# Optimization experiments

Measured on AMD Instinct MI355X. Metric: run time of the kernel, lower is better.

## Reference

```python
import jax, jax.numpy as jnp
import numpy as np

B, T, S, H, E, V, M = 64, 59, 32, 512, 300, 34004, 1024  # batch, dec steps, enc len, hidden, embed, vocab, enc dim (bi)


def setup_inputs() -> dict:
    key = jax.random.key(0)
    ks = jax.random.split(key, 14)
    w = lambda k, sh, sc=0.05: jax.random.normal(k, sh, jnp.float32) * sc
    return dict(
        dec_input=jax.random.randint(ks[0], (B, T), 0, V),
        enc_output=w(ks[1], (B, S, M), 1.0),
        enc_h=w(ks[2], (B, H), 1.0),
        enc_c=w(ks[3], (B, H), 1.0),
        embedding=w(ks[4], (V, E)),
        Wx=w(ks[5], (E + H, 4 * H)),   # LSTM input kernel (input = [emb; prev_attention])
        Uh=w(ks[6], (H, 4 * H)),       # LSTM recurrent kernel
        b=jnp.zeros((4 * H,), jnp.float32),
        Wm=w(ks[7], (M, H)),           # Bahdanau memory layer
        Wq=w(ks[8], (H, H)),           # Bahdanau query layer
        v=w(ks[9], (H,)),              # Bahdanau attention vector
        Wa=w(ks[10], (H + M, H)),      # attention_layer (Dense, no bias)
        Wf=w(ks[11], (H, V)),          # output projection to vocab
        bf=jnp.zeros((V,), jnp.float32),
    )


def reference(dec_input, enc_output, enc_h, enc_c, embedding, Wx, Uh, b, Wm, Wq, v, Wa, Wf, bf):
    # Precompute attention keys once: [B,S,H]
    keys = jnp.einsum('bsm,mh->bsh', enc_output, Wm)
    emb = embedding[dec_input]            # [B,T,E] teacher-forced inputs
    emb_t = jnp.swapaxes(emb, 0, 1)       # [T,B,E]

    def step(carry, x_t):
        h, c, attn = carry
        x = jnp.concatenate([x_t, attn], axis=-1)          # [B,E+H]
        z = x @ Wx + h @ Uh + b                            # [B,4H]
        i, f, g, o = jnp.split(z, 4, axis=-1)              # keras gate order i,f,c,o
        c2 = jax.nn.sigmoid(f) * c + jax.nn.sigmoid(i) * jnp.tanh(g)
        h2 = jax.nn.sigmoid(o) * jnp.tanh(c2)
        # Bahdanau attention: score = v . tanh(keys + Wq q)
        q = h2 @ Wq                                        # [B,H]
        scores = jnp.einsum('h,bsh->bs', v, jnp.tanh(keys + q[:, None, :]))
        align = jax.nn.softmax(scores, axis=-1)            # full memory (seq_len == S)
        ctx = jnp.einsum('bs,bsm->bm', align, enc_output)  # [B,M]
        attn2 = jnp.concatenate([h2, ctx], axis=-1) @ Wa   # attention_layer, [B,H]
        logits = attn2 @ Wf + bf                           # [B,V]
        return (h2, c2, attn2), logits

    init = (enc_h, enc_c, jnp.zeros((B, H), enc_h.dtype))
    _, logits = jax.lax.scan(step, init, emb_t)            # [T,B,V]
    return jnp.swapaxes(logits, 0, 1)                      # [B,T,V]
```

## Files before the change

### kernel.cpp

```cpp
#include <hip/hip_runtime.h>
#include <hip/hip_bf16.h>
#include <hip/hip_fp16.h>
#include <cstdint>
#include <cstddef>

typedef unsigned short u16;
typedef unsigned long long u64;
typedef short s8v __attribute__((ext_vector_type(8)));
typedef float f4v __attribute__((ext_vector_type(4)));
typedef _Float16 f16x2 __attribute__((ext_vector_type(2)));

#define DI __device__ __forceinline__

#if defined(__has_builtin)
#  if __has_builtin(__builtin_amdgcn_fdot2)
#    define HAS_FDOT2 1
#  endif
#endif

DI u16 f2bf(float f){ unsigned u = __float_as_uint(f); u += 0x7fffu + ((u>>16)&1u); return (u16)(u>>16); }
DI float bf2f(u16 h){ return __uint_as_float(((unsigned)h)<<16); }
DI int ocol(int pc){ return ((pc>>3)&3)*512 + (pc>>5)*8 + (pc&7); }
DI int ocol2(int s){ int pc = (s & ~31) | ((s&3)<<3) | ((s>>2)&7); return ocol(pc); }
DI int pc2slot(int pc){ return (pc & ~31) | ((pc&7)<<2) | ((pc>>3)&3); }
DI float sigm(float x){ x = fminf(fmaxf(x,-30.f),30.f); return 1.f/(1.f+__expf(-x)); }
DI float tanhx(float x){ x = fminf(fmaxf(x,-15.f),15.f); float e = __expf(-2.f*x); return (1.f-e)/(1.f+e); }
DI uint4 packh8(const u16* h){
  uint4 r; r.x=(unsigned)h[0]|((unsigned)h[1]<<16); r.y=(unsigned)h[2]|((unsigned)h[3]<<16);
  r.z=(unsigned)h[4]|((unsigned)h[5]<<16); r.w=(unsigned)h[6]|((unsigned)h[7]<<16); return r;
}
DI s8v u4s8(uint4 u){ union{uint4 a; s8v b;} t; t.a=u; return t.b; }

DI float qdot(unsigned w, f16x2 hv, float acc){
#ifdef HAS_FDOT2
  f16x2 wv; __builtin_memcpy(&wv, &w, 4);
  return __builtin_amdgcn_fdot2(wv, hv, acc, false);
#else
  __half2 hp = *reinterpret_cast<const __half2*>(&w);
  return acc + (float)hv[0]*__half2float(hp.x) + (float)hv[1]*__half2float(hp.y);
#endif
}

DI unsigned cohld32(const void* p){
  return __hip_atomic_load((const unsigned*)p, __ATOMIC_RELAXED, __HIP_MEMORY_SCOPE_AGENT);
}
DI u64 cohld64(const void* p){
  return __hip_atomic_load((const u64*)p, __ATOMIC_RELAXED, __HIP_MEMORY_SCOPE_AGENT);
}
DI f4v cohldf4(const float* p){
  u64 lo = cohld64(p);
  u64 hi = cohld64(p + 2);
  f4v r;
  r[0]=__uint_as_float((unsigned)lo); r[1]=__uint_as_float((unsigned)(lo>>32));
  r[2]=__uint_as_float((unsigned)hi); r[3]=__uint_as_float((unsigned)(hi>>32));
  return r;
}
DI void cohst32(void* p, unsigned v){
  __hip_atomic_store((unsigned*)p, v, __ATOMIC_RELAXED, __HIP_MEMORY_SCOPE_AGENT);
}
DI void cohst64(void* p, u64 v){
  __hip_atomic_store((u64*)p, v, __ATOMIC_RELAXED, __HIP_MEMORY_SCOPE_AGENT);
}

__global__ __launch_bounds__(256) void k_build(
    const float* __restrict__ bb, const float* __restrict__ eh, const float* __restrict__ ec,
    const int* __restrict__ dec, const float* __restrict__ enc, const float* __restrict__ emb,
    const float* __restrict__ Wx, const float* __restrict__ Uh, const float* __restrict__ Wm,
    const float* __restrict__ Wq, const float* __restrict__ Wa, const float* __restrict__ Wf,
    float* __restrict__ bp, float* __restrict__ h2X, float* __restrict__ cst,
    float* __restrict__ ctxX, unsigned* __restrict__ flags,
    u16* __restrict__ hhi, u16* __restrict__ hlo, u16* __restrict__ encB,
    u16* __restrict__ wq2, u16* __restrict__ wmT, u16* __restrict__ waT,
    u16* __restrict__ wxtpT, u16* __restrict__ wxaT, u16* __restrict__ buhT,
    u16* __restrict__ waA, u16* __restrict__ embB, u16* __restrict__ WfT){
  __shared__ u16 T[64*72];
  int lb = blockIdx.x, tid = threadIdx.x;
  if (lb < 638){
    int i = lb*256 + tid;
    if (i < 2048) bp[i] = bb[ocol2(i)];
    else if (i < 2048+32768) h2X[i-2048] = eh[i-2048];
    else if (i < 2048+65536) cst[i-34816] = ec[i-34816];
    else if (i < 2048+131072) ctxX[i-67584] = 0.f;
    else if (i < 2048+131072+30208) flags[i-133120] = 0u;
  } else if (lb < 1022){
    int i = (lb-638)*256 + tid; if (i >= 64*1536) return;
    int c = i % 1536;
    float f = (c < 512) ? eh[(i/1536)*512 + c] : 0.f;
    u16 hi = f2bf(f);
    hhi[i] = hi;
    hlo[i] = (c < 512) ? f2bf(f - bf2f(hi)) : (u16)0;
  } else if (lb < 2046){
    int g = (lb-1022)*256 + tid; if (g >= 262144) return;
    const float4* p = (const float4*)(enc + (size_t)g*8);
    float4 a = p[0], b = p[1];
    u16 h[8] = {f2bf(a.x),f2bf(a.y),f2bf(a.z),f2bf(a.w),f2bf(b.x),f2bf(b.y),f2bf(b.z),f2bf(b.w)};
    *(uint4*)&encB[(size_t)g*8] = packh8(h);
  } else if (lb < 3070){
    int g = (lb-2046)*256 + tid; if (g >= 262144) return;
    int h = g>>9, c = g&511;
    __half hf = __float2half(Wq[g]);
    wq2[(size_t)(h>>1)*1024 + (c<<1) + (h&1)] = *reinterpret_cast<u16*>(&hf);
  } else if (lb < 3326){
    int g = (lb-3070)*256 + tid; if (g >= 512*128) return;
    int hcol = g/128, o = g%128;
    u16 h[8];
    #pragma unroll
    for(int j=0;j<8;++j){ int m = o*8+j; h[j]=f2bf(Wm[(size_t)m*512 + hcol]); }
    *(uint4*)&wmT[(size_t)hcol*1024 + o*8] = packh8(h);
  } else if (lb < 3710){
    int g = (lb-3326)*256 + tid; if (g >= 512*192) return;
    int c = g/192, o = g%192;
    u16 h[8];
    #pragma unroll
    for(int j=0;j<8;++j){ int k = o*8+j; h[j]=f2bf(Wa[(size_t)k*512 + c]); }
    *(uint4*)&waT[(size_t)c*1536 + o*8] = packh8(h);
  } else if (lb < 4030){
    int g = (lb-3710)*256 + tid; if (g >= 2048*40) return;
    int pc = g/40, o = g%40; int oc = ocol2(pc);
    u16 h[8];
    #pragma unroll
    for(int j=0;j<8;++j){ int e = o*8+j; float f = (e<300)? Wx[(size_t)e*2048 + oc] : 0.f; h[j]=f2bf(f); }
    *(uint4*)&wxtpT[(size_t)pc*320 + o*8] = packh8(h);
  } else if (lb < 5566){
    int g = (lb-4030)*256 + tid; if (g >= 2048*192) return;
    int pc = g/192, o = g%192; int oc = ocol(pc);
    u16 h[8];
    #pragma unroll
    for(int j=0;j<8;++j){
      int kp = o*8+j; int seg = kp>>9; int jd = kp&511;
      float f = Wx[(size_t)(300+jd)*2048 + oc];
      u16 hi = f2bf(f);
      h[j] = (seg==2) ? f2bf(f - bf2f(hi)) : hi;
    }
    *(uint4*)&wxaT[(size_t)pc*1536 + o*8] = packh8(h);
  } else if (lb < 6590){
    int g = (lb-5566)*256 + tid; if (g >= 2048*128) return;
    int pc = g/128, o = g%128; int oc = ocol(pc);
    u16 h[8];
    #pragma unroll
    for(int j=0;j<8;++j){
      int kp = o*8+j; int r = kp&511;
      float f = Uh[(size_t)r*2048 + oc];
      u16 hi = f2bf(f);
      h[j] = (kp<512) ? hi : f2bf(f - bf2f(hi));
    }
    *(uint4*)&buhT[(size_t)pc*1024 + o*8] = packh8(h);
  } else if (lb < 7742){
    int g = (lb-6590)*256 + tid; if (g >= 1536*192) return;
    int r = g/192, o = g%192;
    u16 h[8];
    #pragma unroll
    for(int j=0;j<8;++j){
      int kp = o*8+j; int seg = kp>>9; int jd = kp&511;
      float f = Wa[(size_t)r*512 + jd];
      u16 hi = f2bf(f);
      h[j] = (seg==1) ? f2bf(f - bf2f(hi)) : hi;
    }
    *(uint4*)&waA[(size_t)r*1536 + o*8] = packh8(h);
  } else if (lb < 8332){
    int g = (lb-7742)*256 + tid; if (g >= 3776*40) return;
    int row = g/40, o = g%40;
    int b = row & 63, t = row >> 6;
    int tok = dec[b*59 + t];
    u16 h[8];
    #pragma unroll
    for(int j=0;j<8;++j){ int k = o*8+j; float f = (k<300)? emb[(size_t)tok*300 + k] : 0.f; h[j]=f2bf(f); }
    *(uint4*)&embB[(size_t)row*320 + o*8] = packh8(h);
  } else {
    int lb2 = lb - 8332;
    int n0 = (lb2 % 532)*64, k0 = (lb2/532)*64;
    int kl = tid>>2, nq = (tid&3)*16;
    u16 h[16];
    if (n0 + 64 <= 34004){
      const float4* p = (const float4*)(Wf + (size_t)(k0+kl)*34004 + n0 + nq);
      #pragma unroll
      for(int q=0;q<4;++q){ float4 f = p[q]; h[q*4+0]=f2bf(f.x); h[q*4+1]=f2bf(f.y); h[q*4+2]=f2bf(f.z); h[q*4+3]=f2bf(f.w); }
    } else {
      #pragma unroll
      for(int j=0;j<16;++j){ int n = n0+nq+j; float f = (n<34004)? Wf[(size_t)(k0+kl)*34004 + n] : 0.f; h[j]=f2bf(f); }
    }
    *(uint4*)&T[kl*72 + nq] = packh8(h);
    *(uint4*)&T[kl*72 + nq + 8] = packh8(h+8);
    __syncthreads();
    int nl = tid>>2, kq = (tid&3)*16;
    int n = n0 + nl;
    if (n < 34004){
      u16 o[16];
      #pragma unroll
      for(int j=0;j<16;++j) o[j] = T[(kq+j)*72 + nl];
      *(uint4*)&WfT[(size_t)n*512 + k0 + kq]     = packh8(o);
      *(uint4*)&WfT[(size_t)n*512 + k0 + kq + 8] = packh8(o+8);
    }
  }
}

__global__ void k_wzcT(const float* __restrict__ wzcT, const float* __restrict__ Uh, u16* __restrict__ dst){
  int g = blockIdx.x*256 + threadIdx.x; if (g >= 2048*384) return;
  int pc = g/384, o = g%384; int oc = ocol(pc);
  u16 h[8];
  #pragma unroll
  for(int j=0;j<8;++j){
    int kp = o*8+j; int r = kp % 1536;
    float f = wzcT[(size_t)pc*1536 + r] + ((r<512) ? Uh[(size_t)r*2048 + oc] : 0.f);
    u16 hi = f2bf(f);
    h[j] = (kp<1536) ? hi : f2bf(f - bf2f(hi));
  }
  *(uint4*)&dst[(size_t)pc*3072 + o*8] = packh8(h);
}

template<int EPI>
DI void gemm_dev(int bx, int by, u16* LSbuf,
    const u16* __restrict__ A, const u16* __restrict__ Bt,
    int M, int N, int K,
    float* __restrict__ Cf, u16* __restrict__ Cb,
    const float* __restrict__ bias, float* __restrict__ Cout){
  u16* Als = LSbuf;
  u16* Bls = LSbuf + 128*40;
  int tid = threadIdx.x;
  int c0 = bx*128, r0 = by*128;
  int wid = tid>>6, wr = wid>>1, wc = wid&1;
  int l15 = tid&15, l4 = (tid>>4)&3;
  f4v acc[4][4];
  #pragma unroll
  for(int m=0;m<4;++m)
  #pragma unroll
  for(int n=0;n<4;++n)
  #pragma unroll
  for(int i=0;i<4;++i) acc[m][n][i] = 0.f;

  int r = tid>>1, hf = tid&1;
  size_t arow = (size_t)min(r0 + r, M-1);
  size_t brow = (size_t)min(c0 + r, N-1);
  const u16* abase = A  + arow*K + hf*16;
  const u16* bbase = Bt + brow*K + hf*16;
  int nk = K >> 5;
  uint4 a0 = ((const uint4*)abase)[0], a1 = ((const uint4*)abase)[1];
  uint4 b0 = ((const uint4*)bbase)[0], b1 = ((const uint4*)bbase)[1];
  for (int ch=0; ch<nk; ++ch){
    __syncthreads();
    *(uint4*)&Als[r*40 + hf*16]     = a0;
    *(uint4*)&Als[r*40 + hf*16 + 8] = a1;
    *(uint4*)&Bls[r*40 + hf*16]     = b0;
    *(uint4*)&Bls[r*40 + hf*16 + 8] = b1;
    __syncthreads();
    if (ch+1 < nk){
      const uint4* ap = (const uint4*)(abase + (ch+1)*32);
      const uint4* bp = (const uint4*)(bbase + (ch+1)*32);
      a0 = ap[0]; a1 = ap[1]; b0 = bp[0]; b1 = bp[1];
    }
    s8v af[4], bfr[4];
    #pragma unroll
    for(int m=0;m<4;++m) af[m]  = *(const s8v*)&Als[(wr*64 + m*16 + l15)*40 + l4*8];
    #pragma unroll
    for(int n=0;n<4;++n) bfr[n] = *(const s8v*)&Bls[(wc*64 + n*16 + l15)*40 + l4*8];
    #pragma unroll
    for(int m=0;m<4;++m)
    #pragma unroll
    for(int n=0;n<4;++n)
      acc[m][n] = __builtin_amdgcn_mfma_f32_16x16x32_bf16(af[m], bfr[n], acc[m][n], 0,0,0);
  }
  __syncthreads();
  float* eps = ((float*)LSbuf) + wid*1024;
  #pragma unroll
  for(int m=0;m<4;++m){
    #pragma unroll
    for(int n=0;n<4;++n)
    #pragma unroll
    for(int i=0;i<4;++i)
      eps[(l4*4 + i)*64 + n*16 + l15] = acc[m][n][i];
    #pragma unroll
    for(int q=0;q<4;++q){
      int row = l4 + q*4;
      f4v v = *(const f4v*)&eps[row*64 + l15*4];
      int gr = r0 + wr*64 + m*16 + row;
      int gc = c0 + wc*64 + l15*4;
      if (gr < M && gc < N){
        if constexpr (EPI==0){
          *(f4v*)&Cf[(size_t)gr*N + gc] = v;
        } else if constexpr (EPI==1){
          f4v bv = *(const f4v*)&bias[gc];
          v += bv;
          *(f4v*)&Cf[(size_t)gr*N + gc] = v;
        } else if constexpr (EPI==2){
          unsigned p0 = ((unsigned)f2bf(v[1])<<16) | f2bf(v[0]);
          unsigned p1 = ((unsigned)f2bf(v[3])<<16) | f2bf(v[2]);
          uint2 pk; pk.x = p0; pk.y = p1;
          *(uint2*)&Cb[(size_t)gr*N + gc] = pk;
        } else {
          f4v bv = *(const f4v*)&bias[gc];
          v += bv;
          int b_ = gr&63, tt = gr>>6;
          *(f4v*)&Cout[((size_t)(b_*59 + tt))*34004 + gc] = v;
        }
      }
    }
  }
}

template<int EPI>
__global__ __launch_bounds__(256,2) void gemm_bf16(
    const u16* __restrict__ A, const u16* __restrict__ Bt,
    int M, int N, int K,
    float* __restrict__ Cf, u16* __restrict__ Cb,
    const float* __restrict__ bias, float* __restrict__ Cout){
  __shared__ u16 LSbuf[2*128*40];
  gemm_dev<EPI>(blockIdx.x, blockIdx.y, LSbuf, A, Bt, M, N, K, Cf, Cb, bias, Cout);
}

__global__ __launch_bounds__(256,2) void k_gemm3(
    const u16* __restrict__ embB, const u16* __restrict__ wxtpT, float* __restrict__ Zemb,
    const float* __restrict__ bp,
    const u16* __restrict__ encB, const u16* __restrict__ wmT, float* __restrict__ keys,
    const u16* __restrict__ wxaT, const u16* __restrict__ waA, float* __restrict__ wzc){
  __shared__ u16 LSbuf[2*128*40];
  int b = blockIdx.x;
  if (b < 480){
    gemm_dev<1>(b%16, b/16, LSbuf, embB, wxtpT, 3776, 2048, 320, Zemb, nullptr, bp, nullptr);
  } else if (b < 544){
    int b2 = b-480;
    gemm_dev<0>(b2%4, b2/4, LSbuf, encB, wmT, 2048, 512, 1024, keys, nullptr, nullptr, nullptr);
  } else {
    int b3 = b-544;
    gemm_dev<0>(b3%12, b3/12, LSbuf, wxaT, waA, 2048, 1536, 1536, wzc, nullptr, nullptr, nullptr);
  }
}

__global__ __launch_bounds__(512,4) void step_fused(
    int t,
    const u16* __restrict__ wzT, const u16* __restrict__ buhT,
    u16* __restrict__ hhi, u16* __restrict__ hlo,
    float* __restrict__ zparts, const float* __restrict__ Zemb,
    float* __restrict__ cst, float* __restrict__ h2X, float* __restrict__ ctxX,
    const u16* __restrict__ wq2, const float* __restrict__ keys,
    const u16* __restrict__ encB, const float* __restrict__ vv,
    unsigned* __restrict__ flags, u16* __restrict__ A2c){
  __shared__ float smem[16384];
  int bid = blockIdx.x, tid = threadIdx.x;
  unsigned* flg = flags + (size_t)t*512;
  int variant = (t==0) ? 0 : 1;

  if (bid < 256){
    int sl = bid>>6, cg = bid&63;
    int pc0 = cg*32;
    int wv = tid>>6, lane = tid&63;
    int l15 = lane&15, l4 = lane>>4;
    const u16* Bt = variant ? wzT : buhT;
    int physK = variant ? 3072 : 1024;
    int CS = variant ? 36 : 12;
    int ck0 = sl*CS, ck1 = ck0 + CS;

    f4v acc[4][2];
    #pragma unroll
    for(int m=0;m<4;++m)
    #pragma unroll
    for(int n=0;n<2;++n)
    #pragma unroll
    for(int i=0;i<4;++i) acc[m][n][i] = 0.f;

    for (int c = ck0 + wv; c < ck1; c += 8){
      int k1 = c*32;
      const u16* ap; int inner, kB;
      if (variant==0){
        inner = k1 & 511;
        ap = ((((k1>>9)&3)==1) ? hlo : hhi);
        kB = (k1 < 1024) ? (k1 & 511) : (k1 - 512);
      } else {
        int sg = k1/1536; inner = k1 - sg*1536;
        ap = (sg==1) ? hlo : hhi;
        kB = (k1 < 3072) ? (k1 % 1536) : (1536 + (k1 - 3072));
      }
      uint4 av[4], bv[2];
      #pragma unroll
      for(int m=0;m<4;++m)
        av[m] = *(const uint4*)(ap + (size_t)(m*16 + l15)*1536 + inner + l4*8);
      #pragma unroll
      for(int n=0;n<2;++n)
        bv[n] = *(const uint4*)(Bt + (size_t)(pc0 + n*16 + l15)*physK + kB + l4*8);
      #pragma unroll
      for(int m=0;m<4;++m){
        s8v am = u4s8(av[m]);
        #pragma unroll
        for(int n=0;n<2;++n)
          acc[m][n] = __builtin_amdgcn_mfma_f32_16x16x32_bf16(am, u4s8(bv[n]), acc[m][n], 0,0,0);
      }
    }
    float* red = smem + wv*2048;
    #pragma unroll
    for(int m=0;m<4;++m)
    #pragma unroll
    for(int n=0;n<2;++n)
    #pragma unroll
    for(int i=0;i<4;++i)
      red[(m*16 + l4*4 + i)*32 + n*16 + l15] = acc[m][n][i];
    __syncthreads();

    int rr = tid>>3, cq = (tid&7)*4;
    f4v s = *(const f4v*)&smem[rr*32 + cq];
    #pragma unroll
    for(int w=1;w<8;++w)
      s += *(const f4v*)&smem[w*2048 + rr*32 + cq];
    float* zp = zparts + (size_t)sl*131072 + (size_t)rr*2048 + pc0 + cq;
    cohst64(&zp[0], (u64)__float_as_uint(s[0]) | ((u64)__float_as_uint(s[1])<<32));
    cohst64(&zp[2], (u64)__float_as_uint(s[2]) | ((u64)__float_as_uint(s[3])<<32));
    asm volatile("s_waitcnt vmcnt(0)" ::: "memory");
    __syncthreads();
    if (tid==0) cohst32(&flg[bid], 1u);

  } else {
    int b = bid - 256;
    int j = tid;
    int base = (j>>3)*32 + (j&7)*4;
    f4v ze = *(const f4v*)&Zemb[(size_t)t*131072 + (size_t)b*2048 + base];
    float cprev = cst[(size_t)b*512 + j];
    float vvj = vv[j];
    if (b == 0){
      if (tid < 256){
        while (cohld32(&flg[tid]) == 0u) __builtin_amdgcn_s_sleep(2);
      }
      __syncthreads();
      if (tid==0) cohst32(&flg[511], 1u);
    } else {
      if (tid==0){
        while (cohld32(&flg[511]) == 0u) __builtin_amdgcn_s_sleep(1);
      }
      __syncthreads();
    }
    asm volatile("" ::: "memory");

    float* zl  = smem;
    float* h2s = smem + 2048;
    float* vs2 = smem + 2560;
    float* qs  = smem + 3072;
    float* qpl = smem + 3584;
    float* scl = smem + 7680;
    float* alw = smem + 7712;
    {
      int p4 = tid*4;
      f4v z0; z0[0]=0.f; z0[1]=0.f; z0[2]=0.f; z0[3]=0.f;
      #pragma unroll
      for(int s2=0; s2<4; ++s2)
        z0 += cohldf4(&zparts[(size_t)s2*131072 + (size_t)b*2048 + p4]);
      #pragma unroll
      for(int e=0;e<4;++e)
        zl[pc2slot(p4+e)] = z0[e];
    }
    __syncthreads();
    {
      f4v s4 = ze + *(const f4v*)&zl[base];
      float c2 = sigm(s4[1])*cprev + sigm(s4[0])*tanhx(s4[2]);
      float h2 = sigm(s4[3])*tanhx(c2);
      cst[(size_t)b*512 + j] = c2;
      h2X[(size_t)(t+1)*32768 + (size_t)b*512 + j] = h2;
      h2s[j] = h2; vs2[j] = vvj;
      u16 hh2 = f2bf(h2);
      hhi[(size_t)b*1536 + j] = hh2;
      hlo[(size_t)b*1536 + j] = f2bf(h2 - bf2f(hh2));
      A2c[((size_t)t*64 + b)*1536 + j] = hh2;
    }
    __syncthreads();
    {
      int c8 = (tid&63)*8, hs = tid>>6;
      float qp[8] = {0,0,0,0,0,0,0,0};
      const u16* wp = wq2 + (size_t)(hs*32)*1024 + c8*2;
      #pragma unroll 4
      for(int i=0;i<32;++i){
        int hp = hs*32 + i;
        f16x2 hv; hv[0] = (_Float16)h2s[2*hp]; hv[1] = (_Float16)h2s[2*hp+1];
        uint4 w0 = *(const uint4*)wp;
        uint4 w1 = *(const uint4*)(wp + 8);
        wp += 1024;
        qp[0]=qdot(w0.x,hv,qp[0]); qp[1]=qdot(w0.y,hv,qp[1]);
        qp[2]=qdot(w0.z,hv,qp[2]); qp[3]=qdot(w0.w,hv,qp[3]);
        qp[4]=qdot(w1.x,hv,qp[4]); qp[5]=qdot(w1.y,hv,qp[5]);
        qp[6]=qdot(w1.z,hv,qp[6]); qp[7]=qdot(w1.w,hv,qp[7]);
      }
      *(float4*)&qpl[hs*512 + c8]     = make_float4(qp[0],qp[1],qp[2],qp[3]);
      *(float4*)&qpl[hs*512 + c8 + 4] = make_float4(qp[4],qp[5],qp[6],qp[7]);
    }
    __syncthreads();
    { float s = 0.f; for(int hs=0; hs<8; ++hs) s += qpl[hs*512 + tid]; qs[tid] = s; }
    __syncthreads();
    {
      int s = tid>>4, hh = tid&15;
      const float4* kb4 = (const float4*)(keys + ((size_t)(b*32 + s))*512 + hh*32);
      float part = 0.f;
      #pragma unroll
      for(int i8=0;i8<8;++i8){
        float4 kv = kb4[i8];
        int h = hh*32 + i8*4;
        part += vs2[h+0]*tanhx(kv.x + qs[h+0]);
        part += vs2[h+1]*tanhx(kv.y + qs[h+1]);
        part += vs2[h+2]*tanhx(kv.z + qs[h+2]);
        part += vs2[h+3]*tanhx(kv.w + qs[h+3]);
      }
      #pragma unroll
      for(int m=1;m<16;m<<=1) part += __shfl_xor(part, m, 64);
      if (hh==0) scl[s] = part;
    }
    __syncthreads();
    if (tid < 32){
      float sc = scl[tid];
      float mx = sc;
      #pragma unroll
      for(int m=1;m<32;m<<=1) mx = fmaxf(mx, __shfl_xor(mx, m, 64));
      float e = __expf(sc - mx);
      float sm = e;
      #pragma unroll
      for(int m=1;m<32;m<<=1) sm += __shfl_xor(sm, m, 64);
      alw[tid] = e/sm;
    }
    __syncthreads();
    {
      const u16* eb = encB + (size_t)b*32768;
      int cc = tid*2;
      float c0 = 0.f, c1 = 0.f;
      for(int s=0;s<32;++s){
        float al = alw[s];
        unsigned ev = *(const unsigned*)&eb[(size_t)s*1024 + cc];
        c0 += al*bf2f((u16)(ev&0xffffu));
        c1 += al*bf2f((u16)(ev>>16));
      }
      float2 co; co.x = c0; co.y = c1;
      *(float2*)&ctxX[(size_t)(t+1)*65536 + (size_t)b*1024 + cc] = co;
      u16 x0 = f2bf(c0), x1 = f2bf(c1);
      unsigned px = (unsigned)x0 | ((unsigned)x1<<16);
      *(unsigned*)&hhi[(size_t)b*1536 + 512 + cc] = px;
      *(unsigned*)&A2c[((size_t)t*64 + b)*1536 + 512 + cc] = px;
      u16 y0 = f2bf(c0 - bf2f(x0)), y1 = f2bf(c1 - bf2f(x1));
      *(unsigned*)&hlo[(size_t)b*1536 + 512 + cc] = (unsigned)y0 | ((unsigned)y1<<16);
    }
  }
}

extern "C" void kernel_launch(void* const* d_in, const int* in_sizes, int n_in,
                              void* d_out, int out_size, void* d_ws, size_t ws_size,
                              hipStream_t stream){
  const int*   dec = (const int*)d_in[0];
  const float* enc = (const float*)d_in[1];
  const float* eh  = (const float*)d_in[2];
  const float* ec  = (const float*)d_in[3];
  const float* emb = (const float*)d_in[4];
  const float* Wx  = (const float*)d_in[5];
  const float* Uh  = (const float*)d_in[6];
  const float* bb  = (const float*)d_in[7];
  const float* Wm  = (const float*)d_in[8];
  const float* Wq  = (const float*)d_in[9];
  const float* vv  = (const float*)d_in[10];
  const float* Wa  = (const float*)d_in[11];
  const float* Wf  = (const float*)d_in[12];
  const float* bf  = (const float*)d_in[13];
  float* out = (float*)d_out;

  char* w = (char*)d_ws; size_t off = 0;
  auto alloc = [&](size_t bytes)->char*{ char* p = w + off; off = (off + bytes + 255) & ~(size_t)255; return p; };
  u16* WfT   = (u16*)alloc((size_t)34004*512*2);
  u16* attn2 = (u16*)alloc((size_t)3776*512*2);
  size_t liveEnd = off;
  const size_t needB = (size_t)131<<20;
  bool fits = (ws_size >= liveEnd + needB);
  char* wb = fits ? (w + liveEnd) : (char*)d_out;
  size_t offb = 0;
  auto allocB = [&](size_t bytes)->char*{ char* p = wb + offb; offb = (offb + bytes + 255) & ~(size_t)255; return p; };

  u16* wzT   = (u16*)allocB((size_t)2048*3072*2);
  u16* buhT  = (u16*)allocB((size_t)2048*1024*2);
  u16* wq2   = (u16*)allocB((size_t)512*512*2);
  u16* waT   = (u16*)allocB((size_t)512*1536*2);
  u16* wmT   = (u16*)allocB((size_t)512*1024*2);
  u16* wxtpT = (u16*)allocB((size_t)2048*320*2);
  u16* wxaT  = (u16*)allocB((size_t)2048*1536*2);
  u16* waA   = (u16*)allocB((size_t)1536*1536*2);
  float* wzc = (float*)allocB((size_t)2048*1536*4);
  u16* embB  = (u16*)allocB((size_t)3776*320*2);
  u16* encB  = (u16*)allocB((size_t)2048*1024*2);
  float* Zemb  = (float*)allocB((size_t)3776*2048*4);
  float* keys  = (float*)allocB((size_t)2048*512*4);
  float* zparts= (float*)allocB((size_t)9*64*2048*4);
  float* h2X   = (float*)allocB((size_t)60*64*512*4);
  float* ctxX  = (float*)allocB((size_t)60*64*1024*4);
  float* cst   = (float*)allocB((size_t)64*512*4);
  float* bp    = (float*)allocB((size_t)2048*4);
  u16* A2c   = (u16*)allocB((size_t)3776*1536*2);
  u16* hhi   = (u16*)allocB((size_t)64*1536*2);
  u16* hlo   = (u16*)allocB((size_t)64*1536*2);
  unsigned* flags = (unsigned*)allocB((size_t)59*512*4);

  k_build<<<12588,256,0,stream>>>(bb, eh, ec, dec, enc, emb, Wx, Uh, Wm, Wq, Wa, Wf,
                                  bp, h2X, cst, ctxX, flags,
                                  hhi, hlo, encB, wq2, wmT, waT,
                                  wxtpT, wxaT, buhT, waA, embB, WfT);

  k_gemm3<<<736,256,0,stream>>>(embB, wxtpT, Zemb, bp, encB, wmT, keys, wxaT, waA, wzc);
  k_wzcT<<<(2048*384+255)/256,256,0,stream>>>(wzc, Uh, wzT);

  for (int t=0; t<59; ++t){
    step_fused<<<320,512,0,stream>>>(t, wzT, buhT, hhi, hlo, zparts, Zemb,
                                     cst, h2X, ctxX, wq2, keys, encB, vv, flags, A2c);
  }

  gemm_bf16<2><<<dim3(4,30),256,0,stream>>>(A2c, waT, 3776, 512, 1536, nullptr, attn2, nullptr, nullptr);
  gemm_bf16<3><<<dim3(266,30),256,0,stream>>>(attn2, WfT, 3776, 34004, 512, nullptr, nullptr, bf, out);
}
```

Before: 1.708 ms.

## Run four decoder steps per launch with flag-based inter-step sync and ring-buffered state

Replaces the 59 per-step launches with launches covering up to four timesteps each. Between steps, blocks synchronize through device-scope flags instead of kernel boundaries, and the hidden-state hi/lo buffers are ring-buffered four deep so a step's readers and the next step's writers do not collide. Unused h2X/ctxX history buffers are dropped, and the cell state stays in registers across the steps of one launch. This cuts launch overhead and kernel-boundary drains, at the cost of spin-waiting, which needs all 320 blocks to be co-resident.

```diff
diff --git a/kernel.cpp b/kernel.cpp
--- a/kernel.cpp
+++ b/kernel.cpp
@@ -67,8 +67,7 @@
     const int* __restrict__ dec, const float* __restrict__ enc, const float* __restrict__ emb,
     const float* __restrict__ Wx, const float* __restrict__ Uh, const float* __restrict__ Wm,
     const float* __restrict__ Wq, const float* __restrict__ Wa, const float* __restrict__ Wf,
-    float* __restrict__ bp, float* __restrict__ h2X, float* __restrict__ cst,
-    float* __restrict__ ctxX, unsigned* __restrict__ flags,
+    float* __restrict__ bp, float* __restrict__ cst, unsigned* __restrict__ flags,
     u16* __restrict__ hhi, u16* __restrict__ hlo, u16* __restrict__ encB,
     u16* __restrict__ wq2, u16* __restrict__ wmT, u16* __restrict__ waT,
     u16* __restrict__ wxtpT, u16* __restrict__ wxaT, u16* __restrict__ buhT,
@@ -78,10 +77,8 @@
   if (lb < 638){
     int i = lb*256 + tid;
     if (i < 2048) bp[i] = bb[ocol2(i)];
-    else if (i < 2048+32768) h2X[i-2048] = eh[i-2048];
-    else if (i < 2048+65536) cst[i-34816] = ec[i-34816];
-    else if (i < 2048+131072) ctxX[i-67584] = 0.f;
-    else if (i < 2048+131072+30208) flags[i-133120] = 0u;
+    else if (i < 2048+32768) cst[i-2048] = ec[i-2048];
+    else if (i < 2048+32768+30208) flags[i-34816] = 0u;
   } else if (lb < 1022){
     int i = (lb-638)*256 + tid; if (i >= 64*1536) return;
     int c = i % 1536;
@@ -325,210 +322,241 @@
   }
 }
 
-__global__ __launch_bounds__(512,4) void step_fused(
-    int t,
+__global__ __launch_bounds__(512,4) void stepN(
+    int t0, int ns,
     const u16* __restrict__ wzT, const u16* __restrict__ buhT,
-    u16* __restrict__ hhi, u16* __restrict__ hlo,
+    u16* __restrict__ hh, u16* __restrict__ hl,
     float* __restrict__ zparts, const float* __restrict__ Zemb,
-    float* __restrict__ cst, float* __restrict__ h2X, float* __restrict__ ctxX,
+    float* __restrict__ cst,
     const u16* __restrict__ wq2, const float* __restrict__ keys,
     const u16* __restrict__ encB, const float* __restrict__ vv,
     unsigned* __restrict__ flags, u16* __restrict__ A2c){
   __shared__ float smem[16384];
   int bid = blockIdx.x, tid = threadIdx.x;
-  unsigned* flg = flags + (size_t)t*512;
-  int variant = (t==0) ? 0 : 1;
 
   if (bid < 256){
     int sl = bid>>6, cg = bid&63;
     int pc0 = cg*32;
     int wv = tid>>6, lane = tid&63;
     int l15 = lane&15, l4 = lane>>4;
-    const u16* Bt = variant ? wzT : buhT;
-    int physK = variant ? 3072 : 1024;
-    int CS = variant ? 36 : 12;
-    int ck0 = sl*CS, ck1 = ck0 + CS;
-
-    f4v acc[4][2];
-    #pragma unroll
-    for(int m=0;m<4;++m)
-    #pragma unroll
-    for(int n=0;n<2;++n)
-    #pragma unroll
-    for(int i=0;i<4;++i) acc[m][n][i] = 0.f;
-
-    for (int c = ck0 + wv; c < ck1; c += 8){
-      int k1 = c*32;
-      const u16* ap; int inner, kB;
-      if (variant==0){
-        inner = k1 & 511;
-        ap = ((((k1>>9)&3)==1) ? hlo : hhi);
-        kB = (k1 < 1024) ? (k1 & 511) : (k1 - 512);
-      } else {
-        int sg = k1/1536; inner = k1 - sg*1536;
-        ap = (sg==1) ? hlo : hhi;
-        kB = (k1 < 3072) ? (k1 % 1536) : (1536 + (k1 - 3072));
-      }
-      uint4 av[4], bv[2];
+    for (int k=0; k<ns; ++k){
+      int t = t0 + k;
+      unsigned* flg = flags + (size_t)t*512;
+      if (k > 0){
+        unsigned* pf = flags + (size_t)(t-1)*512 + 320;
+        if (tid==0){ while (cohld32(pf) == 0u) __builtin_amdgcn_s_sleep(1); }
+        __syncthreads();
+        asm volatile("" ::: "memory");
+      }
+      int variant = (t==0) ? 0 : 1;
+      const u16* hhi = hh + (size_t)((t+3)&3)*98304;
+      const u16* hlo = hl + (size_t)((t+3)&3)*98304;
+      const u16* Bt = variant ? wzT : buhT;
+      int physK = variant ? 3072 : 1024;
+      int CS = variant ? 36 : 12;
+      int ck0 = sl*CS, ck1 = ck0 + CS;
+
+      f4v acc[4][2];
       #pragma unroll
       for(int m=0;m<4;++m)
-        av[m] = *(const uint4*)(ap + (size_t)(m*16 + l15)*1536 + inner + l4*8);
       #pragma unroll
       for(int n=0;n<2;++n)
-        bv[n] = *(const uint4*)(Bt + (size_t)(pc0 + n*16 + l15)*physK + kB + l4*8);
-      #pragma unroll
-      for(int m=0;m<4;++m){
-        s8v am = u4s8(av[m]);
+      #pragma unroll
+      for(int i=0;i<4;++i) acc[m][n][i] = 0.f;
+
+      for (int c = ck0 + wv; c < ck1; c += 8){
+        int k1 = c*32;
+        const u16* ap; int inner, kB;
+        if (variant==0){
+          inner = k1 & 511;
+          ap = ((((k1>>9)&3)==1) ? hlo : hhi);
+          kB = (k1 < 1024) ? (k1 & 511) : (k1 - 512);
+        } else {
+          int sg = k1/1536; inner = k1 - sg*1536;
+          ap = (sg==1) ? hlo : hhi;
+          kB = (k1 < 3072) ? (k1 % 1536) : (1536 + (k1 - 3072));
+        }
+        uint4 av[4], bv[2];
+        #pragma unroll
+        for(int m=0;m<4;++m)
+          av[m] = *(const uint4*)(ap + (size_t)(m*16 + l15)*1536 + inner + l4*8);
         #pragma unroll
         for(int n=0;n<2;++n)
-          acc[m][n] = __builtin_amdgcn_mfma_f32_16x16x32_bf16(am, u4s8(bv[n]), acc[m][n], 0,0,0);
-      }
-    }
-    float* red = smem + wv*2048;
-    #pragma unroll
-    for(int m=0;m<4;++m)
-    #pragma unroll
-    for(int n=0;n<2;++n)
-    #pragma unroll
-    for(int i=0;i<4;++i)
-      red[(m*16 + l4*4 + i)*32 + n*16 + l15] = acc[m][n][i];
-    __syncthreads();
-
-    int rr = tid>>3, cq = (tid&7)*4;
-    f4v s = *(const f4v*)&smem[rr*32 + cq];
-    #pragma unroll
-    for(int w=1;w<8;++w)
-      s += *(const f4v*)&smem[w*2048 + rr*32 + cq];
-    float* zp = zparts + (size_t)sl*131072 + (size_t)rr*2048 + pc0 + cq;
-    cohst64(&zp[0], (u64)__float_as_uint(s[0]) | ((u64)__float_as_uint(s[1])<<32));
-    cohst64(&zp[2], (u64)__float_as_uint(s[2]) | ((u64)__float_as_uint(s[3])<<32));
-    asm volatile("s_waitcnt vmcnt(0)" ::: "memory");
-    __syncthreads();
-    if (tid==0) cohst32(&flg[bid], 1u);
+          bv[n] = *(const uint4*)(Bt + (size_t)(pc0 + n*16 + l15)*physK + kB + l4*8);
+        #pragma unroll
+        for(int m=0;m<4;++m){
+          s8v am = u4s8(av[m]);
+          #pragma unroll
+          for(int n=0;n<2;++n)
+            acc[m][n] = __builtin_amdgcn_mfma_f32_16x16x32_bf16(am, u4s8(bv[n]), acc[m][n], 0,0,0);
+        }
+      }
+      float* red = smem + wv*2048;
+      #pragma unroll
+      for(int m=0;m<4;++m)
+      #pragma unroll
+      for(int n=0;n<2;++n)
+      #pragma unroll
+      for(int i=0;i<4;++i)
+        red[(m*16 + l4*4 + i)*32 + n*16 + l15] = acc[m][n][i];
+      __syncthreads();
+
+      int rr = tid>>3, cq = (tid&7)*4;
+      f4v s = *(const f4v*)&smem[rr*32 + cq];
+      #pragma unroll
+      for(int w=1;w<8;++w)
+        s += *(const f4v*)&smem[w*2048 + rr*32 + cq];
+      float* zp = zparts + (size_t)sl*131072 + (size_t)rr*2048 + pc0 + cq;
+      cohst64(&zp[0], (u64)__float_as_uint(s[0]) | ((u64)__float_as_uint(s[1])<<32));
+      cohst64(&zp[2], (u64)__float_as_uint(s[2]) | ((u64)__float_as_uint(s[3])<<32));
+      asm volatile("s_waitcnt vmcnt(0)" ::: "memory");
+      __syncthreads();
+      if (tid==0) cohst32(&flg[bid], 1u);
+    }
 
   } else {
     int b = bid - 256;
     int j = tid;
     int base = (j>>3)*32 + (j&7)*4;
-    f4v ze = *(const f4v*)&Zemb[(size_t)t*131072 + (size_t)b*2048 + base];
-    float cprev = cst[(size_t)b*512 + j];
     float vvj = vv[j];
-    if (b == 0){
+    float creg = cst[(size_t)b*512 + j];
+
+    for (int k=0; k<ns; ++k){
+      int t = t0 + k;
+      unsigned* flg = flags + (size_t)t*512;
+      u16* hhT = hh + (size_t)(t&3)*98304;
+      u16* hlT = hl + (size_t)(t&3)*98304;
+      f4v ze = *(const f4v*)&Zemb[(size_t)t*131072 + (size_t)b*2048 + base];
+      if (b == 0){
+        if (tid < 256){
+          while (cohld32(&flg[tid]) == 0u) __builtin_amdgcn_s_sleep(2);
+        }
+        __syncthreads();
+        if (tid==0) cohst32(&flg[511], 1u);
+      } else {
+        if (tid==0){
+          while (cohld32(&flg[511]) == 0u) __builtin_amdgcn_s_sleep(1);
+        }
+        __syncthreads();
+      }
+      asm volatile("" ::: "memory");
+
+      float* zl  = smem;
+      float* h2s = smem + 2048;
+      float* vs2 = smem + 2560;
+      float* qs  = smem + 3072;
+      float* qpl = smem + 3584;
+      float* scl = smem + 7680;
+      float* alw = smem + 7712;
+      {
+        int p4 = tid*4;
+        f4v z0; z0[0]=0.f; z0[1]=0.f; z0[2]=0.f; z0[3]=0.f;
+        #pragma unroll
+        for(int s2=0; s2<4; ++s2)
+          z0 += cohldf4(&zparts[(size_t)s2*131072 + (size_t)b*2048 + p4]);
+        #pragma unroll
+        for(int e=0;e<4;++e)
+          zl[pc2slot(p4+e)] = z0[e];
+      }
+      __syncthreads();
+      {
+        f4v s4 = ze + *(const f4v*)&zl[base];
+        float c2 = sigm(s4[1])*creg + sigm(s4[0])*tanhx(s4[2]);
+        float h2 = sigm(s4[3])*tanhx(c2);
+        creg = c2;
+        h2s[j] = h2; vs2[j] = vvj;
+        A2c[((size_t)t*64 + b)*1536 + j] = f2bf(h2);
+      }
+      __syncthreads();
       if (tid < 256){
-        while (cohld32(&flg[tid]) == 0u) __builtin_amdgcn_s_sleep(2);
-      }
-      __syncthreads();
-      if (tid==0) cohst32(&flg[511], 1u);
-    } else {
-      if (tid==0){
-        while (cohld32(&flg[511]) == 0u) __builtin_amdgcn_s_sleep(1);
-      }
-      __syncthreads();
-    }
-    asm volatile("" ::: "memory");
-
-    float* zl  = smem;
-    float* h2s = smem + 2048;
-    float* vs2 = smem + 2560;
-    float* qs  = smem + 3072;
-    float* qpl = smem + 3584;
-    float* scl = smem + 7680;
-    float* alw = smem + 7712;
-    {
-      int p4 = tid*4;
-      f4v z0; z0[0]=0.f; z0[1]=0.f; z0[2]=0.f; z0[3]=0.f;
-      #pragma unroll
-      for(int s2=0; s2<4; ++s2)
-        z0 += cohldf4(&zparts[(size_t)s2*131072 + (size_t)b*2048 + p4]);
-      #pragma unroll
-      for(int e=0;e<4;++e)
-        zl[pc2slot(p4+e)] = z0[e];
-    }
-    __syncthreads();
-    {
-      f4v s4 = ze + *(const f4v*)&zl[base];
-      float c2 = sigm(s4[1])*cprev + sigm(s4[0])*tanhx(s4[2]);
-      float h2 = sigm(s4[3])*tanhx(c2);
-      cst[(size_t)b*512 + j] = c2;
-      h2X[(size_t)(t+1)*32768 + (size_t)b*512 + j] = h2;
-      h2s[j] = h2; vs2[j] = vvj;
-      u16 hh2 = f2bf(h2);
-      hhi[(size_t)b*1536 + j] = hh2;
-      hlo[(size_t)b*1536 + j] = f2bf(h2 - bf2f(hh2));
-      A2c[((size_t)t*64 + b)*1536 + j] = hh2;
-    }
-    __syncthreads();
-    {
-      int c8 = (tid&63)*8, hs = tid>>6;
-      float qp[8] = {0,0,0,0,0,0,0,0};
-      const u16* wp = wq2 + (size_t)(hs*32)*1024 + c8*2;
-      #pragma unroll 4
-      for(int i=0;i<32;++i){
-        int hp = hs*32 + i;
-        f16x2 hv; hv[0] = (_Float16)h2s[2*hp]; hv[1] = (_Float16)h2s[2*hp+1];
-        uint4 w0 = *(const uint4*)wp;
-        uint4 w1 = *(const uint4*)(wp + 8);
-        wp += 1024;
-        qp[0]=qdot(w0.x,hv,qp[0]); qp[1]=qdot(w0.y,hv,qp[1]);
-        qp[2]=qdot(w0.z,hv,qp[2]); qp[3]=qdot(w0.w,hv,qp[3]);
-        qp[4]=qdot(w1.x,hv,qp[4]); qp[5]=qdot(w1.y,hv,qp[5]);
-        qp[6]=qdot(w1.z,hv,qp[6]); qp[7]=qdot(w1.w,hv,qp[7]);
-      }
-      *(float4*)&qpl[hs*512 + c8]     = make_float4(qp[0],qp[1],qp[2],qp[3]);
-      *(float4*)&qpl[hs*512 + c8 + 4] = make_float4(qp[4],qp[5],qp[6],qp[7]);
-    }
-    __syncthreads();
-    { float s = 0.f; for(int hs=0; hs<8; ++hs) s += qpl[hs*512 + tid]; qs[tid] = s; }
-    __syncthreads();
-    {
-      int s = tid>>4, hh = tid&15;
-      const float4* kb4 = (const float4*)(keys + ((size_t)(b*32 + s))*512 + hh*32);
-      float part = 0.f;
-      #pragma unroll
-      for(int i8=0;i8<8;++i8){
-        float4 kv = kb4[i8];
-        int h = hh*32 + i8*4;
-        part += vs2[h+0]*tanhx(kv.x + qs[h+0]);
-        part += vs2[h+1]*tanhx(kv.y + qs[h+1]);
-        part += vs2[h+2]*tanhx(kv.z + qs[h+2]);
-        part += vs2[h+3]*tanhx(kv.w + qs[h+3]);
-      }
-      #pragma unroll
-      for(int m=1;m<16;m<<=1) part += __shfl_xor(part, m, 64);
-      if (hh==0) scl[s] = part;
-    }
-    __syncthreads();
-    if (tid < 32){
-      float sc = scl[tid];
-      float mx = sc;
-      #pragma unroll
-      for(int m=1;m<32;m<<=1) mx = fmaxf(mx, __shfl_xor(mx, m, 64));
-      float e = __expf(sc - mx);
-      float sm = e;
-      #pragma unroll
-      for(int m=1;m<32;m<<=1) sm += __shfl_xor(sm, m, 64);
-      alw[tid] = e/sm;
-    }
-    __syncthreads();
-    {
-      const u16* eb = encB + (size_t)b*32768;
-      int cc = tid*2;
-      float c0 = 0.f, c1 = 0.f;
-      for(int s=0;s<32;++s){
-        float al = alw[s];
-        unsigned ev = *(const unsigned*)&eb[(size_t)s*1024 + cc];
-        c0 += al*bf2f((u16)(ev&0xffffu));
-        c1 += al*bf2f((u16)(ev>>16));
-      }
-      float2 co; co.x = c0; co.y = c1;
-      *(float2*)&ctxX[(size_t)(t+1)*65536 + (size_t)b*1024 + cc] = co;
-      u16 x0 = f2bf(c0), x1 = f2bf(c1);
-      unsigned px = (unsigned)x0 | ((unsigned)x1<<16);
-      *(unsigned*)&hhi[(size_t)b*1536 + 512 + cc] = px;
-      *(unsigned*)&A2c[((size_t)t*64 + b)*1536 + 512 + cc] = px;
-      u16 y0 = f2bf(c0 - bf2f(x0)), y1 = f2bf(c1 - bf2f(x1));
-      *(unsigned*)&hlo[(size_t)b*1536 + 512 + cc] = (unsigned)y0 | ((unsigned)y1<<16);
-    }
+        int j0 = tid*2;
+        float h0 = h2s[j0], h1 = h2s[j0+1];
+        u16 a0 = f2bf(h0), a1 = f2bf(h1);
+        cohst32(&hhT[(size_t)b*1536 + j0], (unsigned)a0 | ((unsigned)a1<<16));
+        u16 b0_ = f2bf(h0 - bf2f(a0)), b1_ = f2bf(h1 - bf2f(a1));
+        cohst32(&hlT[(size_t)b*1536 + j0], (unsigned)b0_ | ((unsigned)b1_<<16));
+      }
+      {
+        int c8 = (tid&63)*8, hs = tid>>6;
+        float qp[8] = {0,0,0,0,0,0,0,0};
+        const u16* wp = wq2 + (size_t)(hs*32)*1024 + c8*2;
+        #pragma unroll 4
+        for(int i=0;i<32;++i){
+          int hp = hs*32 + i;
+          f16x2 hv; hv[0] = (_Float16)h2s[2*hp]; hv[1] = (_Float16)h2s[2*hp+1];
+          uint4 w0 = *(const uint4*)wp;
+          uint4 w1 = *(const uint4*)(wp + 8);
+          wp += 1024;
+          qp[0]=qdot(w0.x,hv,qp[0]); qp[1]=qdot(w0.y,hv,qp[1]);
+          qp[2]=qdot(w0.z,hv,qp[2]); qp[3]=qdot(w0.w,hv,qp[3]);
+          qp[4]=qdot(w1.x,hv,qp[4]); qp[5]=qdot(w1.y,hv,qp[5]);
+          qp[6]=qdot(w1.z,hv,qp[6]); qp[7]=qdot(w1.w,hv,qp[7]);
+        }
+        *(float4*)&qpl[hs*512 + c8]     = make_float4(qp[0],qp[1],qp[2],qp[3]);
+        *(float4*)&qpl[hs*512 + c8 + 4] = make_float4(qp[4],qp[5],qp[6],qp[7]);
+      }
+      __syncthreads();
+      { float s = 0.f; for(int hs=0; hs<8; ++hs) s += qpl[hs*512 + tid]; qs[tid] = s; }
+      __syncthreads();
+      {
+        int s = tid>>4, hh2 = tid&15;
+        const float4* kb4 = (const float4*)(keys + ((size_t)(b*32 + s))*512 + hh2*32);
+        float part = 0.f;
+        #pragma unroll
+        for(int i8=0;i8<8;++i8){
+          float4 kv = kb4[i8];
+          int h = hh2*32 + i8*4;
+          part += vs2[h+0]*tanhx(kv.x + qs[h+0]);
+          part += vs2[h+1]*tanhx(kv.y + qs[h+1]);
+          part += vs2[h+2]*tanhx(kv.z + qs[h+2]);
+          part += vs2[h+3]*tanhx(kv.w + qs[h+3]);
+        }
+        #pragma unroll
+        for(int m=1;m<16;m<<=1) part += __shfl_xor(part, m, 64);
+        if (hh2==0) scl[s] = part;
+      }
+      __syncthreads();
+      if (tid < 32){
+        float sc = scl[tid];
+        float mx = sc;
+        #pragma unroll
+        for(int m=1;m<32;m<<=1) mx = fmaxf(mx, __shfl_xor(mx, m, 64));
+        float e = __expf(sc - mx);
+        float sm = e;
+        #pragma unroll
+        for(int m=1;m<32;m<<=1) sm += __shfl_xor(sm, m, 64);
+        alw[tid] = e/sm;
+      }
+      __syncthreads();
+      {
+        const u16* eb = encB + (size_t)b*32768;
+        int cc = tid*2;
+        float c0 = 0.f, c1 = 0.f;
+        for(int s=0;s<32;++s){
+          float al = alw[s];
+          unsigned ev = *(const unsigned*)&eb[(size_t)s*1024 + cc];
+          c0 += al*bf2f((u16)(ev&0xffffu));
+          c1 += al*bf2f((u16)(ev>>16));
+        }
+        u16 x0 = f2bf(c0), x1 = f2bf(c1);
+        unsigned px = (unsigned)x0 | ((unsigned)x1<<16);
+        cohst32(&hhT[(size_t)b*1536 + 512 + cc], px);
+        *(unsigned*)&A2c[((size_t)t*64 + b)*1536 + 512 + cc] = px;
+        u16 y0 = f2bf(c0 - bf2f(x0)), y1 = f2bf(c1 - bf2f(x1));
+        cohst32(&hlT[(size_t)b*1536 + 512 + cc], (unsigned)y0 | ((unsigned)y1<<16));
+      }
+      asm volatile("s_waitcnt vmcnt(0)" ::: "memory");
+      __syncthreads();
+      if (tid==0) cohst32(&flg[256+b], 1u);
+      if (b == 0){
+        if (tid < 64){
+          while (cohld32(&flg[256+tid]) == 0u) __builtin_amdgcn_s_sleep(1);
+        }
+        __syncthreads();
+        if (tid==0) cohst32(&flg[320], 1u);
+      }
+    }
+    cst[(size_t)b*512 + j] = creg;
   }
 }
 
@@ -576,26 +604,26 @@
   float* Zemb  = (float*)allocB((size_t)3776*2048*4);
   float* keys  = (float*)allocB((size_t)2048*512*4);
   float* zparts= (float*)allocB((size_t)9*64*2048*4);
-  float* h2X   = (float*)allocB((size_t)60*64*512*4);
-  float* ctxX  = (float*)allocB((size_t)60*64*1024*4);
   float* cst   = (float*)allocB((size_t)64*512*4);
   float* bp    = (float*)allocB((size_t)2048*4);
   u16* A2c   = (u16*)allocB((size_t)3776*1536*2);
-  u16* hhi   = (u16*)allocB((size_t)64*1536*2);
-  u16* hlo   = (u16*)allocB((size_t)64*1536*2);
+  u16* hh    = (u16*)allocB((size_t)4*64*1536*2);
+  u16* hl    = (u16*)allocB((size_t)4*64*1536*2);
   unsigned* flags = (unsigned*)allocB((size_t)59*512*4);
 
   k_build<<<12588,256,0,stream>>>(bb, eh, ec, dec, enc, emb, Wx, Uh, Wm, Wq, Wa, Wf,
-                                  bp, h2X, cst, ctxX, flags,
-                                  hhi, hlo, encB, wq2, wmT, waT,
+                                  bp, cst, flags,
+                                  hh + (size_t)3*98304, hl + (size_t)3*98304,
+                                  encB, wq2, wmT, waT,
                                   wxtpT, wxaT, buhT, waA, embB, WfT);
 
   k_gemm3<<<736,256,0,stream>>>(embB, wxtpT, Zemb, bp, encB, wmT, keys, wxaT, waA, wzc);
   k_wzcT<<<(2048*384+255)/256,256,0,stream>>>(wzc, Uh, wzT);
 
-  for (int t=0; t<59; ++t){
-    step_fused<<<320,512,0,stream>>>(t, wzT, buhT, hhi, hlo, zparts, Zemb,
-                                     cst, h2X, ctxX, wq2, keys, encB, vv, flags, A2c);
+  for (int t0=0; t0<59; t0+=4){
+    int ns = (59 - t0 < 4) ? (59 - t0) : 4;
+    stepN<<<320,512,0,stream>>>(t0, ns, wzT, buhT, hh, hl, zparts, Zemb,
+                                cst, wq2, keys, encB, vv, flags, A2c);
   }
 
   gemm_bf16<2><<<dim3(4,30),256,0,stream>>>(A2c, waT, 3776, 512, 1536, nullptr, attn2, nullptr, nullptr);
```

Result: slower. 2.361 ms (+38.2%).
